# Kernel optimization log

Measured on AMD Instinct MI355X. Metric: run time of the kernel, lower is better.

Reference implementation:

```python
import jax, jax.numpy as jnp
import numpy as np

B = 4        # batch_size
S = 128      # input spatial grid size per dim (shape=[128,128,128])
C = 64       # feature channels
N = 500000   # active voxels
K = 2        # kernel_size == stride (non-overlapping sparse max pool)


def setup_inputs() -> dict:
    key = jax.random.key(0)
    kf, kb, ks = jax.random.split(key, 3)
    features = jax.random.normal(kf, (N, C), dtype=jnp.float32)
    b = jax.random.randint(kb, (N, 1), 0, B, dtype=jnp.int32)
    zyx = jax.random.randint(ks, (N, 3), 0, S, dtype=jnp.int32)
    coors = jnp.concatenate([b, zyx], axis=1)  # [N, 4] = (batch, z, y, x)
    return {"features": features, "coors": coors}


def reference(features, coors):
    # Layer 1: sparse 2x2x2/stride-2 max pool == segment-max over output voxel ids.
    S1 = S // K  # 64
    b = coors[:, 0]
    z = coors[:, 1] // K
    y = coors[:, 2] // K
    x = coors[:, 3] // K
    seg = ((b * S1 + z) * S1 + y) * S1 + x  # flat output-site id
    nseg = B * S1 * S1 * S1
    # scatter-max: empty segments become -inf (inactive sites)
    dense = jax.ops.segment_max(features, seg, num_segments=nseg)
    cnt = jax.ops.segment_sum(jnp.ones((N,), jnp.int32), seg, num_segments=nseg)
    mask1 = (cnt > 0).reshape(B, S1, S1, S1)
    dense = dense.reshape(B, S1, S1, S1, C)

    # Layer 2: same pooling on the (now grid-aligned) active sites.
    # -inf at inactive sites makes block-max equal to max over active sites only.
    S2 = S1 // K  # 32
    blocks = dense.reshape(B, S2, K, S2, K, S2, K, C)
    pooled = blocks.max(axis=(2, 4, 6))               # [B, S2, S2, S2, C]
    mask2 = mask1.reshape(B, S2, K, S2, K, S2, K).any(axis=(2, 4, 6))
    out = jnp.where(mask2[..., None], pooled, jnp.float32(0.0))
    return out
```

## Files before the change

### kernel.cpp

```cpp
#include <hip/hip_runtime.h>

#define NB 4
#define S_OUT 32
#define NC 64
#define OUT_CELLS (NB * S_OUT * S_OUT * S_OUT)
#define OUT_ELEMS (OUT_CELLS * NC)
#define CAP 16
#define OVF_CAP 65536


__global__ void fill_kernel(const int4* __restrict__ coors,
                            int* __restrict__ cnt,
                            int* __restrict__ list,
                            int* __restrict__ ovf_cnt,
                            int* __restrict__ ovf,
                            int n_pts) {
    int p = blockIdx.x * blockDim.x + threadIdx.x;
    if (p >= n_pts) return;
    int4 co = coors[p];
    int cell = ((co.x * S_OUT + (co.y >> 2)) * S_OUT + (co.z >> 2)) * S_OUT + (co.w >> 2);
    int slot = atomicAdd(&cnt[cell], 1);
    if (slot < CAP) {
        list[cell * CAP + slot] = p;
    } else {
        int o = atomicAdd(ovf_cnt, 1);
        if (o < OVF_CAP) ovf[o] = p;
    }
}

__global__ __launch_bounds__(256) void gather_kernel(
        const float* __restrict__ features,
        const int* __restrict__ cnt,
        const int* __restrict__ list,
        float* __restrict__ out) {
    int wid  = (blockIdx.x * blockDim.x + threadIdx.x) >> 6;
    int lane = threadIdx.x & 63;
    int cell0 = wid << 2;
    if (cell0 >= OUT_CELLS) return;

    int n = cnt[cell0 + (lane >> 4)];
    int m = n < CAP ? n : CAP;
    int pl = list[(size_t)cell0 * CAP + lane];
    int cl = (lane & 15) << 2;
    int sbase = lane & 48;

    float4 acc = make_float4(-INFINITY, -INFINITY, -INFINITY, -INFINITY);

    #pragma unroll
    for (int s = 0; s < 8; ++s) {
        int p = __shfl(pl, sbase + s);
        bool v = s < m;
        int ps = v ? p : 0;
        const float4 f = *(const float4*)(features + (size_t)ps * NC + cl);
        if (v) {
            acc.x = fmaxf(acc.x, f.x); acc.y = fmaxf(acc.y, f.y);
            acc.z = fmaxf(acc.z, f.z); acc.w = fmaxf(acc.w, f.w);
        }
    }
    if (m > 8) {
        for (int s = 8; s < m; ++s) {
            int p = __shfl(pl, sbase + s);
            const float4 f = *(const float4*)(features + (size_t)p * NC + cl);
            acc.x = fmaxf(acc.x, f.x); acc.y = fmaxf(acc.y, f.y);
            acc.z = fmaxf(acc.z, f.z); acc.w = fmaxf(acc.w, f.w);
        }
    }
    if (n == 0) acc = make_float4(0.f, 0.f, 0.f, 0.f);
    *(float4*)(out + (size_t)cell0 * NC + (size_t)lane * 4) = acc;
}

__device__ __forceinline__ void atomicMaxFloat(float* addr, float val) {
    unsigned* ua = (unsigned*)addr;
    unsigned old = *ua;
    while (true) {
        float f = __uint_as_float(old);
        if (f >= val) break;
        unsigned assumed = old;
        old = atomicCAS(ua, assumed, __float_as_uint(val));
        if (old == assumed) break;
    }
}

__global__ void ovf_kernel(const float* __restrict__ features,
                           const int4* __restrict__ coors,
                           const int* __restrict__ ovf_cnt,
                           const int* __restrict__ ovf,
                           float* __restrict__ out) {
    int lane = threadIdx.x & 63;
    int wid = (blockIdx.x * blockDim.x + threadIdx.x) >> 6;
    int nw = (gridDim.x * blockDim.x) >> 6;
    int n = *ovf_cnt;
    if (n > OVF_CAP) n = OVF_CAP;
    for (int i = wid; i < n; i += nw) {
        int p = ovf[i];
        int4 co = coors[p];
        int cell = ((co.x * S_OUT + (co.y >> 2)) * S_OUT + (co.z >> 2)) * S_OUT + (co.w >> 2);
        atomicMaxFloat(&out[(size_t)cell * NC + lane], features[(size_t)p * NC + lane]);
    }
}


__device__ __forceinline__ unsigned flip_f(float f) {
    unsigned u = __float_as_uint(f);
    return (u & 0x80000000u) ? ~u : (u | 0x80000000u);
}
__device__ __forceinline__ float unflip_f(unsigned u) {
    unsigned v = (u & 0x80000000u) ? (u & 0x7FFFFFFFu) : ~u;
    return __uint_as_float(v);
}

__global__ void init_kernel(uint4* __restrict__ out4, int n4) {
    int i = blockIdx.x * blockDim.x + threadIdx.x;
    int stride = gridDim.x * blockDim.x;
    uint4 z = make_uint4(0u, 0u, 0u, 0u);
    for (; i < n4; i += stride) out4[i] = z;
}

__global__ void scatter_kernel(const float* __restrict__ features,
                               const int4* __restrict__ coors,
                               unsigned* __restrict__ acc, int n_pts) {
    int gid = blockIdx.x * blockDim.x + threadIdx.x;
    int p = gid >> 6;
    int c = threadIdx.x & 63;
    if (p >= n_pts) return;
    int4 co = coors[p];
    int cell = ((co.x * S_OUT + (co.y >> 2)) * S_OUT + (co.z >> 2)) * S_OUT + (co.w >> 2);
    atomicMax(acc + (size_t)cell * NC + c, flip_f(features[(size_t)p * NC + c]));
}

__global__ void finalize_kernel(unsigned* __restrict__ acc, int n) {
    int i = blockIdx.x * blockDim.x + threadIdx.x;
    int stride = gridDim.x * blockDim.x;
    for (; i < n; i += stride) {
        unsigned u = acc[i];
        ((float*)acc)[i] = (u == 0u) ? 0.0f : unflip_f(u);
    }
}

extern "C" void kernel_launch(void* const* d_in, const int* in_sizes, int n_in,
                              void* d_out, int out_size, void* d_ws, size_t ws_size,
                              hipStream_t stream) {
    const float* features = (const float*)d_in[0];
    const int4*  coors    = (const int4*)d_in[1];
    int n_pts = in_sizes[0] / NC;

    const size_t off_cnt  = 0;
    const size_t cnt_b    = (size_t)OUT_CELLS * 4;
    const size_t off_ovfc = cnt_b;
    const size_t off_ovf  = off_ovfc + 256;
    const size_t off_list = off_ovf + (size_t)OVF_CAP * 4;
    const size_t need     = off_list + (size_t)OUT_CELLS * CAP * 4;

    if (ws_size >= need) {
        char* ws = (char*)d_ws;
        int* cnt     = (int*)(ws + off_cnt);
        int* ovf_cnt = (int*)(ws + off_ovfc);
        int* ovf     = (int*)(ws + off_ovf);
        int* list    = (int*)(ws + off_list);
        float* out   = (float*)d_out;

        hipMemsetAsync(ws, 0, off_ovfc + 4, stream);

        {
            int block = 256;
            int grid = (n_pts + block - 1) / block;
            fill_kernel<<<grid, block, 0, stream>>>(coors, cnt, list, ovf_cnt, ovf, n_pts);
        }
        {
            int block = 256;
            int grid = (OUT_CELLS / 4 * 64) / block;
            gather_kernel<<<grid, block, 0, stream>>>(features, cnt, list, out);
        }
        ovf_kernel<<<16, 256, 0, stream>>>(features, coors, ovf_cnt, ovf, out);
    } else {
        unsigned* acc = (unsigned*)d_out;
        init_kernel<<<2048, 256, 0, stream>>>((uint4*)d_out, OUT_ELEMS / 4);
        int grid = (n_pts * 64 + 255) / 256;
        scatter_kernel<<<grid, 256, 0, stream>>>(features, coors, acc, n_pts);
        finalize_kernel<<<2048, 256, 0, stream>>>(acc, OUT_ELEMS);
    }
}
```

Baseline: 64.63 us.

## Fold overflow handling into persistent gather kernel with prefetch and nontemporal stores

Turns the gather kernel into a persistent grid-stride kernel on a fixed grid. It prefetches the next group's counts and list entries while the current group is processed. The separate overflow kernel is removed: a wave whose cells exceeded the list capacity scans the overflow list inline, so one launch and its atomic CAS loop go away. Output is written with nontemporal stores to avoid polluting the cache, at the cost of possibly long serial overflow scans if many cells overflow.

```diff
diff --git a/kernel.cpp b/kernel.cpp
--- a/kernel.cpp
+++ b/kernel.cpp
@@ -5,8 +5,11 @@
 #define NC 64
 #define OUT_CELLS (NB * S_OUT * S_OUT * S_OUT)
 #define OUT_ELEMS (OUT_CELLS * NC)
+#define NGROUPS (OUT_CELLS / 4)
 #define CAP 16
 #define OVF_CAP 65536
+
+typedef float floatx4 __attribute__((ext_vector_type(4)));
 
 
 __global__ void fill_kernel(const int4* __restrict__ coors,
@@ -30,72 +33,77 @@
 
 __global__ __launch_bounds__(256) void gather_kernel(
         const float* __restrict__ features,
+        const int4* __restrict__ coors,
         const int* __restrict__ cnt,
         const int* __restrict__ list,
+        const int* __restrict__ ovf_cnt,
+        const int* __restrict__ ovf,
         float* __restrict__ out) {
-    int wid  = (blockIdx.x * blockDim.x + threadIdx.x) >> 6;
-    int lane = threadIdx.x & 63;
-    int cell0 = wid << 2;
-    if (cell0 >= OUT_CELLS) return;
+    const int lane  = threadIdx.x & 63;
+    const int wid   = (blockIdx.x * blockDim.x + threadIdx.x) >> 6;
+    const int nw    = (gridDim.x * blockDim.x) >> 6;
+    const int cl    = (lane & 15) << 2;
+    const int sbase = lane & 48;
+    const int qsel  = lane >> 4;
 
-    int n = cnt[cell0 + (lane >> 4)];
-    int m = n < CAP ? n : CAP;
-    int pl = list[(size_t)cell0 * CAP + lane];
-    int cl = (lane & 15) << 2;
-    int sbase = lane & 48;
+    int g = wid;
+    if (g >= NGROUPS) return;
 
-    float4 acc = make_float4(-INFINITY, -INFINITY, -INFINITY, -INFINITY);
+    int n_pf  = cnt[(g << 2) + qsel];
+    int pl_pf = list[((size_t)g << 6) + lane];
 
-    #pragma unroll
-    for (int s = 0; s < 8; ++s) {
-        int p = __shfl(pl, sbase + s);
-        bool v = s < m;
-        int ps = v ? p : 0;
-        const float4 f = *(const float4*)(features + (size_t)ps * NC + cl);
-        if (v) {
-            acc.x = fmaxf(acc.x, f.x); acc.y = fmaxf(acc.y, f.y);
-            acc.z = fmaxf(acc.z, f.z); acc.w = fmaxf(acc.w, f.w);
+    while (true) {
+        int n  = n_pf;
+        int pl = pl_pf;
+        int gn = g + nw;
+        if (gn < NGROUPS) {
+            n_pf  = cnt[(gn << 2) + qsel];
+            pl_pf = list[((size_t)gn << 6) + lane];
         }
-    }
-    if (m > 8) {
-        for (int s = 8; s < m; ++s) {
+
+        int m = n < CAP ? n : CAP;
+        float4 acc = make_float4(-INFINITY, -INFINITY, -INFINITY, -INFINITY);
+
+        #pragma unroll
+        for (int s = 0; s < 8; ++s) {
             int p = __shfl(pl, sbase + s);
-            const float4 f = *(const float4*)(features + (size_t)p * NC + cl);
-            acc.x = fmaxf(acc.x, f.x); acc.y = fmaxf(acc.y, f.y);
-            acc.z = fmaxf(acc.z, f.z); acc.w = fmaxf(acc.w, f.w);
+            bool v = s < m;
+            int ps = v ? p : 0;
+            const float4 f = *(const float4*)(features + (size_t)ps * NC + cl);
+            if (v) {
+                acc.x = fmaxf(acc.x, f.x); acc.y = fmaxf(acc.y, f.y);
+                acc.z = fmaxf(acc.z, f.z); acc.w = fmaxf(acc.w, f.w);
+            }
         }
-    }
-    if (n == 0) acc = make_float4(0.f, 0.f, 0.f, 0.f);
-    *(float4*)(out + (size_t)cell0 * NC + (size_t)lane * 4) = acc;
-}
+        if (m > 8) {
+            for (int s = 8; s < m; ++s) {
+                int p = __shfl(pl, sbase + s);
+                const float4 f = *(const float4*)(features + (size_t)p * NC + cl);
+                acc.x = fmaxf(acc.x, f.x); acc.y = fmaxf(acc.y, f.y);
+                acc.z = fmaxf(acc.z, f.z); acc.w = fmaxf(acc.w, f.w);
+            }
+        }
+        if (__builtin_expect(__any(n > CAP), 0)) {
+            int mycell = (g << 2) + qsel;
+            int novf = *ovf_cnt;
+            if (novf > OVF_CAP) novf = OVF_CAP;
+            for (int i = 0; i < novf; ++i) {
+                int p = ovf[i];
+                int4 co = coors[p];
+                int cellp = ((co.x * S_OUT + (co.y >> 2)) * S_OUT + (co.z >> 2)) * S_OUT + (co.w >> 2);
+                if (n > CAP && cellp == mycell) {
+                    const float4 f = *(const float4*)(features + (size_t)p * NC + cl);
+                    acc.x = fmaxf(acc.x, f.x); acc.y = fmaxf(acc.y, f.y);
+                    acc.z = fmaxf(acc.z, f.z); acc.w = fmaxf(acc.w, f.w);
+                }
+            }
+        }
+        if (n == 0) acc = make_float4(0.f, 0.f, 0.f, 0.f);
+        floatx4 accv = { acc.x, acc.y, acc.z, acc.w };
+        __builtin_nontemporal_store(accv, (floatx4*)(out + ((size_t)g << 8) + (size_t)lane * 4));
 
-__device__ __forceinline__ void atomicMaxFloat(float* addr, float val) {
-    unsigned* ua = (unsigned*)addr;
-    unsigned old = *ua;
-    while (true) {
-        float f = __uint_as_float(old);
-        if (f >= val) break;
-        unsigned assumed = old;
-        old = atomicCAS(ua, assumed, __float_as_uint(val));
-        if (old == assumed) break;
-    }
-}
-
-__global__ void ovf_kernel(const float* __restrict__ features,
-                           const int4* __restrict__ coors,
-                           const int* __restrict__ ovf_cnt,
-                           const int* __restrict__ ovf,
-                           float* __restrict__ out) {
-    int lane = threadIdx.x & 63;
-    int wid = (blockIdx.x * blockDim.x + threadIdx.x) >> 6;
-    int nw = (gridDim.x * blockDim.x) >> 6;
-    int n = *ovf_cnt;
-    if (n > OVF_CAP) n = OVF_CAP;
-    for (int i = wid; i < n; i += nw) {
-        int p = ovf[i];
-        int4 co = coors[p];
-        int cell = ((co.x * S_OUT + (co.y >> 2)) * S_OUT + (co.z >> 2)) * S_OUT + (co.w >> 2);
-        atomicMaxFloat(&out[(size_t)cell * NC + lane], features[(size_t)p * NC + lane]);
+        if (gn >= NGROUPS) break;
+        g = gn;
     }
 }
 
@@ -159,7 +167,7 @@
         int* list    = (int*)(ws + off_list);
         float* out   = (float*)d_out;
 
-        hipMemsetAsync(ws, 0, off_ovfc + 4, stream);
+        (void)hipMemsetAsync(ws, 0, off_ovfc + 4, stream);
 
         {
             int block = 256;
@@ -168,10 +176,10 @@
         }
         {
             int block = 256;
-            int grid = (OUT_CELLS / 4 * 64) / block;
-            gather_kernel<<<grid, block, 0, stream>>>(features, cnt, list, out);
+            int grid = 2048;
+            gather_kernel<<<grid, block, 0, stream>>>(features, coors, cnt, list,
+                                                      ovf_cnt, ovf, out);
         }
-        ovf_kernel<<<16, 256, 0, stream>>>(features, coors, ovf_cnt, ovf, out);
     } else {
         unsigned* acc = (unsigned*)d_out;
         init_kernel<<<2048, 256, 0, stream>>>((uint4*)d_out, OUT_ELEMS / 4);
```

Measured after the change: 63.95 us. Within noise of the previous version (-1.0%).
